# Kernel optimization log

Hardware: AMD Instinct MI355X
Metric: run time of the kernel (lower is better)

## Reference

```python
import jax, jax.numpy as jnp
import numpy as np

EPS = 1e-5

def mean_normalization(feat):
    # per (batch, channel) statistics over spatial dims, unbiased variance (torch default)
    mean = jnp.mean(feat, axis=(2, 3), keepdims=True)
    var = jnp.var(feat, axis=(2, 3), keepdims=True, ddof=1)
    return (feat - mean) / jnp.sqrt(var + EPS)

def setup_inputs() -> dict:
    key = jax.random.key(0)
    ks = jax.random.split(key, 8)
    B, C, H, W = 4, 512, 64, 64
    fan = np.sqrt(6.0 / (C + C))  # xavier_uniform gain=1 for 1x1 conv
    return {
        "content_feat": jax.random.normal(ks[0], (B, C, H, W), jnp.float32),
        "style_feat": jax.random.normal(ks[1], (B, C, H, W), jnp.float32),
        "Wq": jax.random.uniform(ks[2], (C, C), jnp.float32, -fan, fan),
        "bq": jax.random.uniform(ks[3], (C,), jnp.float32, 0.0, 1.0),
        "Wk": jax.random.uniform(ks[4], (C, C), jnp.float32, -fan, fan),
        "bk": jax.random.uniform(ks[5], (C,), jnp.float32, 0.0, 1.0),
        "Wv": jax.random.uniform(ks[6], (C, C), jnp.float32, -fan, fan),
        "bv": jax.random.uniform(ks[7], (C,), jnp.float32, 0.0, 1.0),
    }

def reference(content_feat, style_feat, Wq, bq, Wk, bk, Wv, bv):
    B, C, H, W = content_feat.shape
    N = H * W
    # 1x1 convs == channel-mixing GEMMs
    Q = jnp.einsum('oc,bchw->bohw', Wq, mean_normalization(content_feat)) + bq[None, :, None, None]
    K = jnp.einsum('oc,bchw->bohw', Wk, mean_normalization(style_feat)) + bk[None, :, None, None]
    V = jnp.einsum('oc,bchw->bohw', Wv, style_feat) + bv[None, :, None, None]
    Q = Q.reshape(B, C, N)              # [B, C, Nq]
    K = K.reshape(B, C, N)              # [B, C, Nk]
    V = V.reshape(B, C, N)              # [B, C, Nk]
    # scores[b, n, m] = Q^T K  (no 1/sqrt(d) scaling, per original)
    scores = jnp.einsum('bcn,bcm->bnm', Q, K)
    A = jax.nn.softmax(scores, axis=-1)             # [B, Nq, Nk]
    Out = jnp.einsum('bcm,bnm->bcn', V, A)          # V @ A^T
    return Out.reshape(B, C, H, W)
```

## Files before the change

### kernel.cpp

```cpp
#include <hip/hip_runtime.h>

typedef _Float16 f16;
typedef _Float16 f16x4 __attribute__((ext_vector_type(4)));
typedef _Float16 f16x8 __attribute__((ext_vector_type(8)));
typedef float f32x4 __attribute__((ext_vector_type(4)));

#define MFMA16(a, b, c) __builtin_amdgcn_mfma_f32_16x16x32_f16(a, b, c, 0, 0, 0)

__global__ __launch_bounds__(256) void stats_kernel(
    const float* __restrict__ content, const float* __restrict__ style,
    float* __restrict__ mu, float* __restrict__ rs)
{
    int bid = blockIdx.x;
    int tensor = bid >> 11;
    int row = bid & 2047;
    const float* src = (tensor ? style : content) + (size_t)row * 4096;
    int t = threadIdx.x;
    float s = 0.f, ss = 0.f;
    for (int i = t; i < 1024; i += 256) {
        float4 v = reinterpret_cast<const float4*>(src)[i];
        s  += v.x + v.y + v.z + v.w;
        ss += v.x * v.x + v.y * v.y + v.z * v.z + v.w * v.w;
    }
    for (int off = 32; off > 0; off >>= 1) {
        s  += __shfl_down(s, off);
        ss += __shfl_down(ss, off);
    }
    __shared__ float sb[4], ssb[4];
    int wv = t >> 6;
    if ((t & 63) == 0) { sb[wv] = s; ssb[wv] = ss; }
    __syncthreads();
    if (t == 0) {
        float S  = sb[0] + sb[1] + sb[2] + sb[3];
        float SS = ssb[0] + ssb[1] + ssb[2] + ssb[3];
        float m  = S * (1.f / 4096.f);
        float var = (SS - 4096.f * m * m) * (1.f / 4095.f);
        mu[bid] = m;
        rs[bid] = rsqrtf(var + 1e-5f);
    }
}

__global__ __launch_bounds__(256) void wcvt_kernel(
    const float* __restrict__ Wq, const float* __restrict__ Wk,
    const float* __restrict__ Wv, f16* __restrict__ Wh)
{
    int p = blockIdx.y;
    const float* W = (p == 0 ? Wq : (p == 1 ? Wk : Wv));
    f16* dst = Wh + (size_t)p * 262144;
    int base = blockIdx.x * 256 + threadIdx.x;
#pragma unroll
    for (int i = 0; i < 8; ++i) {
        int e4 = i * 8192 + base;
        float4 v = reinterpret_cast<const float4*>(W)[e4];
        f16x4 pk;
        pk[0] = (f16)v.x; pk[1] = (f16)v.y; pk[2] = (f16)v.z; pk[3] = (f16)v.w;
        reinterpret_cast<f16x4*>(dst)[e4] = pk;
    }
}

__global__ __launch_bounds__(512, 3) void qkv_kernel(
    const float* __restrict__ content, const float* __restrict__ style,
    const f16* __restrict__ Wh,
    const float* __restrict__ bq, const float* __restrict__ bk,
    const float* __restrict__ bv,
    const float* __restrict__ mu, const float* __restrict__ rs,
    f16* __restrict__ Qt, f16* __restrict__ Kt, f16* __restrict__ Vc)
{
    int nb = blockIdx.x;
    int y  = blockIdx.y;
    int b = y / 3, p = y % 3;
    int n0 = nb * 64;
    const float* X    = (p == 0 ? content : style) + (size_t)b * 512 * 4096;
    const f16*   Wp   = Wh + (size_t)p * 262144;
    const float* bias = (p == 0 ? bq : (p == 1 ? bk : bv));
    const float* muT  = mu + (p == 0 ? 0 : 2048) + b * 512;
    const float* rsT  = rs + (p == 0 ? 0 : 2048) + b * 512;
    bool norm = (p < 2);

    __shared__ __align__(16) f16 Xt[64][520];

    int t = threadIdx.x;
    int lane = t & 63, w = t >> 6;
    int lg = lane >> 4, li = lane & 15;

#pragma unroll
    for (int i = 0; i < 16; ++i) {
        int c0 = i * 32 + w * 4;
        float x0 = X[(size_t)(c0 + 0) * 4096 + n0 + lane];
        float x1 = X[(size_t)(c0 + 1) * 4096 + n0 + lane];
        float x2 = X[(size_t)(c0 + 2) * 4096 + n0 + lane];
        float x3 = X[(size_t)(c0 + 3) * 4096 + n0 + lane];
        f16x4 pk;
        if (norm) {
            pk[0] = (f16)((x0 - muT[c0 + 0]) * rsT[c0 + 0]);
            pk[1] = (f16)((x1 - muT[c0 + 1]) * rsT[c0 + 1]);
            pk[2] = (f16)((x2 - muT[c0 + 2]) * rsT[c0 + 2]);
            pk[3] = (f16)((x3 - muT[c0 + 3]) * rsT[c0 + 3]);
        } else {
            pk[0] = (f16)x0; pk[1] = (f16)x1; pk[2] = (f16)x2; pk[3] = (f16)x3;
        }
        *reinterpret_cast<f16x4*>(&Xt[lane][c0]) = pk;
    }
    __syncthreads();

    f32x4 acc[4][4];
#pragma unroll
    for (int i = 0; i < 4; ++i)
#pragma unroll
        for (int j = 0; j < 4; ++j)
#pragma unroll
            for (int e = 0; e < 4; ++e) acc[i][j][e] = 0.f;

    const f16* wbase = Wp + (size_t)(w * 64 + li) * 512 + lg * 8;
    for (int kk = 0; kk < 16; ++kk) {
        f16x8 xf[4], wf[4];
#pragma unroll
        for (int jn = 0; jn < 4; ++jn)
            xf[jn] = *reinterpret_cast<const f16x8*>(&Xt[jn * 16 + li][kk * 32 + lg * 8]);
#pragma unroll
        for (int io = 0; io < 4; ++io)
            wf[io] = *reinterpret_cast<const f16x8*>(wbase + (size_t)io * 16 * 512 + kk * 32);
        if (p < 2) {
#pragma unroll
            for (int io = 0; io < 4; ++io)
#pragma unroll
                for (int jn = 0; jn < 4; ++jn)
                    acc[io][jn] = MFMA16(wf[io], xf[jn], acc[io][jn]);
        } else {
#pragma unroll
            for (int jn = 0; jn < 4; ++jn)
#pragma unroll
                for (int io = 0; io < 4; ++io)
                    acc[jn][io] = MFMA16(xf[jn], wf[io], acc[jn][io]);
        }
    }

    if (p < 2) {
        f16* dst = (p == 0 ? Qt : Kt) + (size_t)b * 4096 * 512;
#pragma unroll
        for (int io = 0; io < 4; ++io) {
            int ob = w * 64 + io * 16 + lg * 4;
            float4 bb = *reinterpret_cast<const float4*>(bias + ob);
#pragma unroll
            for (int jn = 0; jn < 4; ++jn) {
                int n = n0 + jn * 16 + li;
                f16x4 pk;
                pk[0] = (f16)(acc[io][jn][0] + bb.x);
                pk[1] = (f16)(acc[io][jn][1] + bb.y);
                pk[2] = (f16)(acc[io][jn][2] + bb.z);
                pk[3] = (f16)(acc[io][jn][3] + bb.w);
                *reinterpret_cast<f16x4*>(dst + (size_t)n * 512 + ob) = pk;
            }
        }
    } else {
#pragma unroll
        for (int io = 0; io < 4; ++io) {
            int o = w * 64 + io * 16 + li;
            float bb = bias[o];
            f16* dst = Vc + ((size_t)b * 512 + o) * 4096;
#pragma unroll
            for (int jn = 0; jn < 4; ++jn) {
                int n = n0 + jn * 16 + lg * 4;
                f16x4 pk;
#pragma unroll
                for (int e = 0; e < 4; ++e) pk[e] = (f16)(acc[jn][io][e] + bb);
                *reinterpret_cast<f16x4*>(dst + n) = pk;
            }
        }
    }
}

__global__ __launch_bounds__(768, 3) void attn_kernel(
    const f16* __restrict__ Qt, const f16* __restrict__ Kt,
    const f16* __restrict__ Vc, float* __restrict__ out)
{
    int bid = blockIdx.x;
    int orig = (bid & 7) * 32 + (bid >> 3);
    int b = orig >> 6;
    int n0 = (orig & 63) * 64;

    int t = threadIdx.x;
    int lane = t & 63, w = t >> 6;
    int lg = lane >> 4, li = lane & 15;

    __shared__ __align__(16) f16 Km[2][64][528];
    __shared__ __align__(16) f16 Pl[2][64][68];
    __shared__ __align__(16) float Rrow[2][64];
    __shared__ __align__(16) float Lrow[64];
    __shared__ int Rflag[2][4];

    const f16* Qb = Qt + (size_t)b * 4096 * 512;
    const f16* Kb = Kt + (size_t)b * 4096 * 512;
    const f16* Vb = Vc + (size_t)b * 512 * 4096;

    if (w < 4) {
        int j = w;
        f16x8 qf[16];
#pragma unroll
        for (int kk = 0; kk < 16; ++kk)
            qf[kk] = *reinterpret_cast<const f16x8*>(
                Qb + (size_t)(n0 + j * 16 + li) * 512 + kk * 32 + lg * 8);

#define STAGEK(TILE)                                                           \
        {                                                                      \
            int _db = (TILE) & 1;                                              \
            _Pragma("unroll")                                                  \
            for (int r = 0; r < 16; ++r) {                                     \
                const f16* _gs = Kb + ((size_t)(TILE) * 64 + j * 16 + r) * 512 \
                                 + lane * 8;                                   \
                __builtin_amdgcn_global_load_lds(                              \
                    (const __attribute__((address_space(1))) void*)_gs,        \
                    (__attribute__((address_space(3))) void*)&Km[_db][j * 16 + r][0], \
                    16, 0, 0);                                                 \
            }                                                                  \
        }

        STAGEK(0);
        float Mreg = -3.4e38f, Lreg = 0.f;
        __syncthreads();

        for (int it = 0; it <= 64; ++it) {
            if (it <= 63) {
                int cur = it & 1;
                if (it < 63) STAGEK(it + 1);

                f32x4 s[4];
#pragma unroll
                for (int mg = 0; mg < 4; ++mg)
#pragma unroll
                    for (int e = 0; e < 4; ++e) s[mg][e] = 0.f;
                __builtin_amdgcn_s_setprio(1);
#pragma unroll
                for (int kk = 0; kk < 16; ++kk) {
#pragma unroll
                    for (int mg = 0; mg < 4; ++mg) {
                        f16x8 kf = *reinterpret_cast<const f16x8*>(
                            &Km[cur][mg * 16 + li][kk * 32 + lg * 8]);
                        s[mg] = MFMA16(kf, qf[kk], s[mg]);
                    }
                }
                __builtin_amdgcn_s_setprio(0);

                float mx = s[0][0];
#pragma unroll
                for (int mg = 0; mg < 4; ++mg)
#pragma unroll
                    for (int e = 0; e < 4; ++e) mx = fmaxf(mx, s[mg][e]);
                mx = fmaxf(mx, __shfl_xor(mx, 16));
                mx = fmaxf(mx, __shfl_xor(mx, 32));
                bool needR = (mx - Mreg) > 4.0f;
                float Mnew = needR ? mx : Mreg;
                float r = needR ? __expf(Mreg - Mnew) : 1.f;
                float p[4][4];
                float sum = 0.f;
#pragma unroll
                for (int mg = 0; mg < 4; ++mg)
#pragma unroll
                    for (int e = 0; e < 4; ++e) {
                        p[mg][e] = __expf(s[mg][e] - Mnew);
                        sum += p[mg][e];
                    }
                sum += __shfl_xor(sum, 16);
                sum += __shfl_xor(sum, 32);
                Lreg = Lreg * r + sum;
                Mreg = Mnew;

#pragma unroll
                for (int mg = 0; mg < 4; ++mg) {
                    f16x4 pk;
#pragma unroll
                    for (int e = 0; e < 4; ++e) pk[e] = (f16)p[mg][e];
                    *reinterpret_cast<f16x4*>(&Pl[cur][j * 16 + li][mg * 16 + lg * 4]) = pk;
                }
                if (lg == 0) Rrow[cur][j * 16 + li] = r;
                int any = __any(needR);
                if (lane == 0) Rflag[cur][j] = any;
                if (it == 63 && lg == 0) Lrow[j * 16 + li] = Lreg;
            }
            __syncthreads();
        }
#undef STAGEK
    } else {
        int pw = w - 4;
        int c0 = pw * 64;
        f32x4 acc[4][4];
#pragma unroll
        for (int fn = 0; fn < 4; ++fn)
#pragma unroll
            for (int fc = 0; fc < 4; ++fc)
#pragma unroll
                for (int e = 0; e < 4; ++e) acc[fn][fc][e] = 0.f;
        f16x8 vfr[4][2];

        __syncthreads();

        for (int it = 0; it <= 64; ++it) {
            if (it >= 1) {
                int pp = (it - 1) & 1;
                if (Rflag[pp][0] | Rflag[pp][1] | Rflag[pp][2] | Rflag[pp][3]) {
#pragma unroll
                    for (int fn = 0; fn < 4; ++fn) {
                        f32x4 rv = *reinterpret_cast<const f32x4*>(&Rrow[pp][fn * 16 + lg * 4]);
#pragma unroll
                        for (int fc = 0; fc < 4; ++fc)
#pragma unroll
                            for (int e = 0; e < 4; ++e) acc[fn][fc][e] *= rv[e];
                    }
                }
                __builtin_amdgcn_s_setprio(1);
#pragma unroll
                for (int fn = 0; fn < 4; ++fn) {
                    f16x8 af0 = *reinterpret_cast<const f16x8*>(&Pl[pp][fn * 16 + li][lg * 8]);
                    f16x8 af1 = *reinterpret_cast<const f16x8*>(&Pl[pp][fn * 16 + li][32 + lg * 8]);
#pragma unroll
                    for (int fc = 0; fc < 4; ++fc) {
                        acc[fn][fc] = MFMA16(af0, vfr[fc][0], acc[fn][fc]);
                        acc[fn][fc] = MFMA16(af1, vfr[fc][1], acc[fn][fc]);
                    }
                }
                __builtin_amdgcn_s_setprio(0);
            }
            if (it <= 63) {
                const f16* vs = Vb + (size_t)(c0 + li) * 4096 + it * 64 + lg * 8;
#pragma unroll
                for (int fc = 0; fc < 4; ++fc) {
                    vfr[fc][0] = *reinterpret_cast<const f16x8*>(vs + (size_t)fc * 16 * 4096);
                    vfr[fc][1] = *reinterpret_cast<const f16x8*>(vs + (size_t)fc * 16 * 4096 + 32);
                }
            }
            __syncthreads();
        }

        float* ob = out + (size_t)b * 512 * 4096;
#pragma unroll
        for (int fn = 0; fn < 4; ++fn) {
            f32x4 lv = *reinterpret_cast<const f32x4*>(&Lrow[fn * 16 + lg * 4]);
            f32x4 linv;
#pragma unroll
            for (int e = 0; e < 4; ++e) linv[e] = 1.f / lv[e];
#pragma unroll
            for (int fc = 0; fc < 4; ++fc) {
                int c = c0 + fc * 16 + li;
                f32x4 o4;
#pragma unroll
                for (int e = 0; e < 4; ++e) o4[e] = acc[fn][fc][e] * linv[e];
                *reinterpret_cast<f32x4*>(ob + (size_t)c * 4096 + n0 + fn * 16 + lg * 4) = o4;
            }
        }
    }
}

extern "C" void kernel_launch(void* const* d_in, const int* in_sizes, int n_in,
                              void* d_out, int out_size, void* d_ws, size_t ws_size,
                              hipStream_t stream)
{
    const float* content = (const float*)d_in[0];
    const float* style   = (const float*)d_in[1];
    const float* Wq = (const float*)d_in[2];
    const float* bq = (const float*)d_in[3];
    const float* Wk = (const float*)d_in[4];
    const float* bk = (const float*)d_in[5];
    const float* Wv = (const float*)d_in[6];
    const float* bv = (const float*)d_in[7];
    float* out = (float*)d_out;

    const size_t TEN = (size_t)4 * 4096 * 512;
    f16* Qt = (f16*)d_ws;
    f16* Kt = Qt + TEN;
    f16* Vc = Kt + TEN;
    float* mu = (float*)(Vc + TEN);
    float* rs = mu + 4096;
    f16* Wh = (f16*)(rs + 4096);

    hipLaunchKernelGGL(stats_kernel, dim3(4096), dim3(256), 0, stream,
                       content, style, mu, rs);
    hipLaunchKernelGGL(wcvt_kernel, dim3(32, 3), dim3(256), 0, stream,
                       Wq, Wk, Wv, Wh);
    hipLaunchKernelGGL(qkv_kernel, dim3(64, 12), dim3(512), 0, stream,
                       content, style, Wh, bq, bk, bv, mu, rs, Qt, Kt, Vc);
    hipLaunchKernelGGL(attn_kernel, dim3(256), dim3(768), 0, stream,
                       Qt, Kt, Vc, out);
}
```

Before: 250.6 us.

## Use 32x32 MFMA for QK^T with two score waves and double-buffer V loads

The score computation in the attention kernel moves from four waves using 16x16x32 MFMAs to two waves using 32x32x16 MFMAs. Each wave now owns 32 query rows and splits the K-dim into two accumulator chains to hide MFMA latency. The block shrinks from 768 to 640 threads, and the launch bounds change from (768,3) to (640,2). The PV waves ping-pong two V register buffers so the global load for the next tile is issued before the current MFMAs, giving more overlap. This costs higher register pressure and a different softmax reduction layout, and halving the score waves may serialize the score stage.

Result: slower. 459.0 us (+83.2%).

```diff
diff --git a/kernel.cpp b/kernel.cpp
--- a/kernel.cpp
+++ b/kernel.cpp
@@ -4,8 +4,10 @@
 typedef _Float16 f16x4 __attribute__((ext_vector_type(4)));
 typedef _Float16 f16x8 __attribute__((ext_vector_type(8)));
 typedef float f32x4 __attribute__((ext_vector_type(4)));
+typedef float f32x16 __attribute__((ext_vector_type(16)));
 
 #define MFMA16(a, b, c) __builtin_amdgcn_mfma_f32_16x16x32_f16(a, b, c, 0, 0, 0)
+#define MFMA32(a, b, c) __builtin_amdgcn_mfma_f32_32x32x16_f16(a, b, c, 0, 0, 0)
 
 __global__ __launch_bounds__(256) void stats_kernel(
     const float* __restrict__ content, const float* __restrict__ style,
@@ -170,7 +172,7 @@
     }
 }
 
-__global__ __launch_bounds__(768, 3) void attn_kernel(
+__global__ __launch_bounds__(640, 2) void attn_kernel(
     const f16* __restrict__ Qt, const f16* __restrict__ Kt,
     const f16* __restrict__ Vc, float* __restrict__ out)
 {
@@ -182,35 +184,36 @@
     int t = threadIdx.x;
     int lane = t & 63, w = t >> 6;
     int lg = lane >> 4, li = lane & 15;
+    int li32 = lane & 31, hi = lane >> 5;
 
     __shared__ __align__(16) f16 Km[2][64][528];
     __shared__ __align__(16) f16 Pl[2][64][68];
     __shared__ __align__(16) float Rrow[2][64];
     __shared__ __align__(16) float Lrow[64];
-    __shared__ int Rflag[2][4];
+    __shared__ int Rflag[2][2];
 
     const f16* Qb = Qt + (size_t)b * 4096 * 512;
     const f16* Kb = Kt + (size_t)b * 4096 * 512;
     const f16* Vb = Vc + (size_t)b * 512 * 4096;
 
-    if (w < 4) {
+    if (w < 2) {
         int j = w;
-        f16x8 qf[16];
-#pragma unroll
-        for (int kk = 0; kk < 16; ++kk)
+        f16x8 qf[32];
+#pragma unroll
+        for (int kk = 0; kk < 32; ++kk)
             qf[kk] = *reinterpret_cast<const f16x8*>(
-                Qb + (size_t)(n0 + j * 16 + li) * 512 + kk * 32 + lg * 8);
+                Qb + (size_t)(n0 + j * 32 + li32) * 512 + kk * 16 + hi * 8);
 
 #define STAGEK(TILE)                                                           \
         {                                                                      \
             int _db = (TILE) & 1;                                              \
             _Pragma("unroll")                                                  \
-            for (int r = 0; r < 16; ++r) {                                     \
-                const f16* _gs = Kb + ((size_t)(TILE) * 64 + j * 16 + r) * 512 \
+            for (int r = 0; r < 32; ++r) {                                     \
+                const f16* _gs = Kb + ((size_t)(TILE) * 64 + j * 32 + r) * 512 \
                                  + lane * 8;                                   \
                 __builtin_amdgcn_global_load_lds(                              \
                     (const __attribute__((address_space(1))) void*)_gs,        \
-                    (__attribute__((address_space(3))) void*)&Km[_db][j * 16 + r][0], \
+                    (__attribute__((address_space(3))) void*)&Km[_db][j * 32 + r][0], \
                     16, 0, 0);                                                 \
             }                                                                  \
         }
@@ -224,64 +227,71 @@
                 int cur = it & 1;
                 if (it < 63) STAGEK(it + 1);
 
-                f32x4 s[4];
-#pragma unroll
-                for (int mg = 0; mg < 4; ++mg)
-#pragma unroll
-                    for (int e = 0; e < 4; ++e) s[mg][e] = 0.f;
+                f32x16 s00, s01, s10, s11;
+#pragma unroll
+                for (int e = 0; e < 16; ++e) { s00[e] = 0.f; s01[e] = 0.f; s10[e] = 0.f; s11[e] = 0.f; }
                 __builtin_amdgcn_s_setprio(1);
 #pragma unroll
                 for (int kk = 0; kk < 16; ++kk) {
-#pragma unroll
-                    for (int mg = 0; mg < 4; ++mg) {
-                        f16x8 kf = *reinterpret_cast<const f16x8*>(
-                            &Km[cur][mg * 16 + li][kk * 32 + lg * 8]);
-                        s[mg] = MFMA16(kf, qf[kk], s[mg]);
-                    }
+                    f16x8 a0h0 = *reinterpret_cast<const f16x8*>(&Km[cur][li32][kk * 16 + hi * 8]);
+                    f16x8 a0h1 = *reinterpret_cast<const f16x8*>(&Km[cur][li32][(kk + 16) * 16 + hi * 8]);
+                    f16x8 a1h0 = *reinterpret_cast<const f16x8*>(&Km[cur][32 + li32][kk * 16 + hi * 8]);
+                    f16x8 a1h1 = *reinterpret_cast<const f16x8*>(&Km[cur][32 + li32][(kk + 16) * 16 + hi * 8]);
+                    s00 = MFMA32(a0h0, qf[kk], s00);
+                    s01 = MFMA32(a0h1, qf[kk + 16], s01);
+                    s10 = MFMA32(a1h0, qf[kk], s10);
+                    s11 = MFMA32(a1h1, qf[kk + 16], s11);
                 }
                 __builtin_amdgcn_s_setprio(0);
-
-                float mx = s[0][0];
-#pragma unroll
-                for (int mg = 0; mg < 4; ++mg)
-#pragma unroll
-                    for (int e = 0; e < 4; ++e) mx = fmaxf(mx, s[mg][e]);
-                mx = fmaxf(mx, __shfl_xor(mx, 16));
-                mx = fmaxf(mx, __shfl_xor(mx, 32));
+                f32x16 st0, st1;
+#pragma unroll
+                for (int e = 0; e < 16; ++e) { st0[e] = s00[e] + s01[e]; st1[e] = s10[e] + s11[e]; }
+
+                float tm[16];
+#pragma unroll
+                for (int e = 0; e < 16; ++e) tm[e] = fmaxf(st0[e], st1[e]);
+#pragma unroll
+                for (int d = 8; d > 0; d >>= 1)
+#pragma unroll
+                    for (int e = 0; e < d; ++e) tm[e] = fmaxf(tm[e], tm[e + d]);
+                float mx = fmaxf(tm[0], __shfl_xor(tm[0], 32));
                 bool needR = (mx - Mreg) > 4.0f;
                 float Mnew = needR ? mx : Mreg;
                 float r = needR ? __expf(Mreg - Mnew) : 1.f;
-                float p[4][4];
-                float sum = 0.f;
-#pragma unroll
-                for (int mg = 0; mg < 4; ++mg)
-#pragma unroll
-                    for (int e = 0; e < 4; ++e) {
-                        p[mg][e] = __expf(s[mg][e] - Mnew);
-                        sum += p[mg][e];
-                    }
-                sum += __shfl_xor(sum, 16);
-                sum += __shfl_xor(sum, 32);
+                float p0[16], p1[16];
+                float ts[16];
+#pragma unroll
+                for (int e = 0; e < 16; ++e) {
+                    p0[e] = __expf(st0[e] - Mnew);
+                    p1[e] = __expf(st1[e] - Mnew);
+                    ts[e] = p0[e] + p1[e];
+                }
+#pragma unroll
+                for (int d = 8; d > 0; d >>= 1)
+#pragma unroll
+                    for (int e = 0; e < d; ++e) ts[e] += ts[e + d];
+                float sum = ts[0] + __shfl_xor(ts[0], 32);
                 Lreg = Lreg * r + sum;
                 Mreg = Mnew;
 
 #pragma unroll
-                for (int mg = 0; mg < 4; ++mg) {
-                    f16x4 pk;
-#pragma unroll
-                    for (int e = 0; e < 4; ++e) pk[e] = (f16)p[mg][e];
-                    *reinterpret_cast<f16x4*>(&Pl[cur][j * 16 + li][mg * 16 + lg * 4]) = pk;
+                for (int g = 0; g < 4; ++g) {
+                    f16x4 pk0, pk1;
+#pragma unroll
+                    for (int e = 0; e < 4; ++e) { pk0[e] = (f16)p0[g * 4 + e]; pk1[e] = (f16)p1[g * 4 + e]; }
+                    *reinterpret_cast<f16x4*>(&Pl[cur][j * 32 + li32][g * 8 + hi * 4]) = pk0;
+                    *reinterpret_cast<f16x4*>(&Pl[cur][j * 32 + li32][32 + g * 8 + hi * 4]) = pk1;
                 }
-                if (lg == 0) Rrow[cur][j * 16 + li] = r;
+                if (lane < 32) Rrow[cur][j * 32 + lane] = r;
                 int any = __any(needR);
                 if (lane == 0) Rflag[cur][j] = any;
-                if (it == 63 && lg == 0) Lrow[j * 16 + li] = Lreg;
+                if (it == 63 && lane < 32) Lrow[j * 32 + lane] = Lreg;
             }
             __syncthreads();
         }
 #undef STAGEK
     } else {
-        int pw = w - 4;
+        int pw = w - 2;
         int c0 = pw * 64;
         f32x4 acc[4][4];
 #pragma unroll
@@ -290,46 +300,52 @@
             for (int fc = 0; fc < 4; ++fc)
 #pragma unroll
                 for (int e = 0; e < 4; ++e) acc[fn][fc][e] = 0.f;
-        f16x8 vfr[4][2];
+        f16x8 vA[4][2], vB[4][2];
 
         __syncthreads();
 
-        for (int it = 0; it <= 64; ++it) {
-            if (it >= 1) {
-                int pp = (it - 1) & 1;
-                if (Rflag[pp][0] | Rflag[pp][1] | Rflag[pp][2] | Rflag[pp][3]) {
-#pragma unroll
-                    for (int fn = 0; fn < 4; ++fn) {
-                        f32x4 rv = *reinterpret_cast<const f32x4*>(&Rrow[pp][fn * 16 + lg * 4]);
-#pragma unroll
-                        for (int fc = 0; fc < 4; ++fc)
-#pragma unroll
-                            for (int e = 0; e < 4; ++e) acc[fn][fc][e] *= rv[e];
-                    }
-                }
-                __builtin_amdgcn_s_setprio(1);
-#pragma unroll
-                for (int fn = 0; fn < 4; ++fn) {
-                    f16x8 af0 = *reinterpret_cast<const f16x8*>(&Pl[pp][fn * 16 + li][lg * 8]);
-                    f16x8 af1 = *reinterpret_cast<const f16x8*>(&Pl[pp][fn * 16 + li][32 + lg * 8]);
-#pragma unroll
-                    for (int fc = 0; fc < 4; ++fc) {
-                        acc[fn][fc] = MFMA16(af0, vfr[fc][0], acc[fn][fc]);
-                        acc[fn][fc] = MFMA16(af1, vfr[fc][1], acc[fn][fc]);
-                    }
-                }
-                __builtin_amdgcn_s_setprio(0);
-            }
-            if (it <= 63) {
-                const f16* vs = Vb + (size_t)(c0 + li) * 4096 + it * 64 + lg * 8;
-#pragma unroll
-                for (int fc = 0; fc < 4; ++fc) {
-                    vfr[fc][0] = *reinterpret_cast<const f16x8*>(vs + (size_t)fc * 16 * 4096);
-                    vfr[fc][1] = *reinterpret_cast<const f16x8*>(vs + (size_t)fc * 16 * 4096 + 32);
-                }
-            }
-            __syncthreads();
-        }
+#define PVBODY(IT, VCON, VLD)                                                  \
+        {                                                                      \
+            if ((IT) <= 63) {                                                  \
+                const f16* vs = Vb + (size_t)(c0 + li) * 4096 + (IT) * 64 + lg * 8; \
+                _Pragma("unroll")                                              \
+                for (int fc = 0; fc < 4; ++fc) {                               \
+                    VLD[fc][0] = *reinterpret_cast<const f16x8*>(vs + (size_t)fc * 16 * 4096); \
+                    VLD[fc][1] = *reinterpret_cast<const f16x8*>(vs + (size_t)fc * 16 * 4096 + 32); \
+                }                                                              \
+            }                                                                  \
+            if ((IT) >= 1) {                                                   \
+                int pp = ((IT) - 1) & 1;                                       \
+                if (Rflag[pp][0] | Rflag[pp][1]) {                             \
+                    _Pragma("unroll")                                          \
+                    for (int fn = 0; fn < 4; ++fn) {                           \
+                        f32x4 rv = *reinterpret_cast<const f32x4*>(&Rrow[pp][fn * 16 + lg * 4]); \
+                        _Pragma("unroll")                                      \
+                        for (int fc = 0; fc < 4; ++fc)                         \
+                            for (int e = 0; e < 4; ++e) acc[fn][fc][e] *= rv[e]; \
+                    }                                                          \
+                }                                                              \
+                __builtin_amdgcn_s_setprio(1);                                 \
+                _Pragma("unroll")                                              \
+                for (int fn = 0; fn < 4; ++fn) {                               \
+                    f16x8 af0 = *reinterpret_cast<const f16x8*>(&Pl[pp][fn * 16 + li][lg * 8]); \
+                    f16x8 af1 = *reinterpret_cast<const f16x8*>(&Pl[pp][fn * 16 + li][32 + lg * 8]); \
+                    _Pragma("unroll")                                          \
+                    for (int fc = 0; fc < 4; ++fc) {                           \
+                        acc[fn][fc] = MFMA16(af0, VCON[fc][0], acc[fn][fc]);   \
+                        acc[fn][fc] = MFMA16(af1, VCON[fc][1], acc[fn][fc]);   \
+                    }                                                          \
+                }                                                              \
+                __builtin_amdgcn_s_setprio(0);                                 \
+            }                                                                  \
+            __syncthreads();                                                   \
+        }
+
+        for (int it2 = 0; it2 <= 64; it2 += 2) {
+            PVBODY(it2, vB, vA)
+            if (it2 + 1 <= 64) PVBODY(it2 + 1, vA, vB)
+        }
+#undef PVBODY
 
         float* ob = out + (size_t)b * 512 * 4096;
 #pragma unroll
@@ -378,6 +394,6 @@
                        Wq, Wk, Wv, Wh);
     hipLaunchKernelGGL(qkv_kernel, dim3(64, 12), dim3(512), 0, stream,
                        content, style, Wh, bq, bk, bv, mu, rs, Qt, Kt, Vc);
-    hipLaunchKernelGGL(attn_kernel, dim3(256), dim3(768), 0, stream,
+    hipLaunchKernelGGL(attn_kernel, dim3(256), dim3(640), 0, stream,
                        Qt, Kt, Vc, out);
 }
```
